# Performance work log

Hardware: AMD Instinct MI355X
Metric: run time of the kernel (lower is better)

The kernel has to match this reference:

```python
import jax, jax.numpy as jnp
import numpy as np


def setup_inputs() -> dict:
    key = jax.random.key(0)
    k1, k2, k3, k4 = jax.random.split(key, 4)
    N, T, F = 8192, 128, 9
    M_s = 256
    merged = jax.random.normal(k1, (N, T, F), dtype=jnp.float32)
    input1 = jax.random.normal(k2, (N, T, F), dtype=jnp.float32)
    samples = jax.random.normal(k3, (N, M_s), dtype=jnp.float32)
    labels = jax.random.randint(k4, (N,), 0, 10, dtype=jnp.int32)
    return {"merged": merged, "input1": input1, "samples": samples, "labels": labels}


def reference(merged, input1, samples, labels):
    # Pairwise squared distances S_ij = sum_k (s_i - s_j)^2 / M_s, computed via
    # the Gram-matrix identity instead of materializing the [N, N, M_s] tensor.
    M_s = samples.shape[1]
    sq = jnp.sum(samples * samples, axis=-1)                 # [N]
    gram = jnp.einsum('im,jm->ij', samples, samples)         # [N, N]
    S_ij = (sq[:, None] + sq[None, :] - 2.0 * gram) / jnp.float32(M_s)
    same = (labels[:, None] == labels[None, :]).astype(jnp.float32)
    term2 = jnp.mean(jnp.maximum(0.0, (1.0 - same) * (1.0 - S_ij)))
    L_label = 10.0 * jnp.mean(same * S_ij) + 10.0 * term2
    return L_label
```

## Files before the change

kernel.cpp:

```cpp
#include <hip/hip_runtime.h>
#include <hip/hip_bf16.h>

#define NROWS 8192
#define KDIM  256
#define NT    64
#define NBLK  (NT * (NT + 1) / 2)
#define GRID  256

typedef __attribute__((ext_vector_type(4))) float f32x4;

#define GLD(gp, lp)                                                            \
  __builtin_amdgcn_global_load_lds(                                            \
      (const __attribute__((address_space(1))) void*)(gp),                     \
      (__attribute__((address_space(3))) void*)(lp), 16, 0, 0)

__global__ void prep_kernel(const float* __restrict__ samples,
                            unsigned char* __restrict__ sf8,
                            float* __restrict__ sq,
                            float* __restrict__ accg) {
  int row = blockIdx.x, t = threadIdx.x;
  float2 v2 = ((const float2*)samples)[(size_t)row * 128 + t];
  int pk = __builtin_amdgcn_cvt_pk_fp8_f32(v2.x, v2.y, 0, false);
  ((unsigned short*)sf8)[(size_t)row * 128 + t] = (unsigned short)(pk & 0xffff);
  float p = v2.x * v2.x + v2.y * v2.y;
#pragma unroll
  for (int off = 32; off; off >>= 1) p += __shfl_down(p, off);
  __shared__ float ws2[2];
  if ((t & 63) == 0) ws2[t >> 6] = p;
  __syncthreads();
  if (t == 0) sq[row] = ws2[0] + ws2[1];
  if (row == 0 && t < 2) accg[t] = 0.0f;
}

__device__ inline void decode_tile(int b, int& bi, int& bj) {
  float disc = (2.0f * NT + 1.0f) * (2.0f * NT + 1.0f) - 8.0f * (float)b;
  bi = (int)(((2.0f * NT + 1.0f) - sqrtf(disc)) * 0.5f);
  if (bi < 0) bi = 0;
  if (bi > NT - 1) bi = NT - 1;
  while (bi > 0 && (bi * NT - bi * (bi - 1) / 2) > b) --bi;
  while (((bi + 1) * NT - (bi + 1) * bi / 2) <= b) ++bi;
  bj = bi + (b - (bi * NT - bi * (bi - 1) / 2));
}

__global__ __launch_bounds__(512, 1) void pair_kernel(
    const unsigned char* __restrict__ sf8, const float* __restrict__ sq,
    const int* __restrict__ labels, float* __restrict__ accg) {

  __shared__ __align__(16) unsigned char As[2][128 * 256];
  __shared__ __align__(16) unsigned char Bs[2][128 * 256];
  __shared__ float red[16];

  int t = threadIdx.x;
  int lane = t & 63;
  int w = t >> 6;
  int wm = w >> 1, wn = w & 1;
  int lr = lane >> 4, pc = lane & 15;
  int r = lane & 15;
  int kq = (lane >> 4) >> 1;
  int hf = ((lane >> 4) & 1) * 8;
  int q4 = (lane >> 4) * 4;
  int cl = lane & 15;

  float s1t = 0.f, s2t = 0.f;

  auto stage = [&](int bi_, int bj_, int buf) {
    int rA = bi_ * 128, rB = bj_ * 128;
#pragma unroll
    for (int p = 0; p < 4; ++p) {
      int region = p * 8 + w;
      int rr = region * 4 + lr;
      int c = pc ^ (rr & 15);
      GLD(sf8 + (size_t)(rA + rr) * KDIM + c * 16, &As[buf][region * 1024]);
      GLD(sf8 + (size_t)(rB + rr) * KDIM + c * 16, &Bs[buf][region * 1024]);
    }
  };

  int tile = blockIdx.x;
  int bi, bj;
  decode_tile(tile, bi, bj);
  stage(bi, bj, 0);
  int cur = 0;

  while (tile < NBLK) {
    int ntile = tile + GRID;
    int nbi = 0, nbj = 0;
    bool have_next = ntile < NBLK;
    if (have_next) decode_tile(ntile, nbi, nbj);

    __syncthreads();

    int rowA0 = bi * 128, rowB0 = bj * 128;
    float sqa[8], sqb[4];
    int laa[8], lab[4];
#pragma unroll
    for (int i = 0; i < 2; i++)
#pragma unroll
      for (int q = 0; q < 4; q++) {
        int gr = rowA0 + wm * 32 + i * 16 + q4 + q;
        sqa[i * 4 + q] = sq[gr];
        laa[i * 4 + q] = labels[gr];
      }
#pragma unroll
    for (int j = 0; j < 4; j++) {
      int gc = rowB0 + wn * 64 + j * 16 + cl;
      sqb[j] = sq[gc];
      lab[j] = labels[gc];
    }

    if (have_next) stage(nbi, nbj, cur ^ 1);

    f32x4 acc[2][4];
#pragma unroll
    for (int i = 0; i < 2; i++)
#pragma unroll
      for (int j = 0; j < 4; j++) acc[i][j] = (f32x4){0.f, 0.f, 0.f, 0.f};

#pragma unroll
    for (int kc = 0; kc < 8; ++kc) {
      long af[2], bfr[4];
#pragma unroll
      for (int i = 0; i < 2; i++) {
        int m = wm * 32 + i * 16 + r;
        af[i] = *(const long*)(&As[cur][m * 256 + (((kc * 2 + kq) ^ r) * 16) + hf]);
      }
#pragma unroll
      for (int j = 0; j < 4; j++) {
        int n = wn * 64 + j * 16 + r;
        bfr[j] = *(const long*)(&Bs[cur][n * 256 + (((kc * 2 + kq) ^ r) * 16) + hf]);
      }
#pragma unroll
      for (int i = 0; i < 2; i++)
#pragma unroll
        for (int j = 0; j < 4; j++)
          acc[i][j] = __builtin_amdgcn_mfma_f32_16x16x32_fp8_fp8(
              af[i], bfr[j], acc[i][j], 0, 0, 0);
    }

    float s1 = 0.f, s2 = 0.f;
#pragma unroll
    for (int j = 0; j < 4; j++) {
#pragma unroll
      for (int i = 0; i < 2; i++) {
#pragma unroll
        for (int q = 0; q < 4; q++) {
          float S = (sqa[i * 4 + q] + sqb[j] - 2.0f * acc[i][j][q]) *
                    (1.0f / 256.0f);
          if (laa[i * 4 + q] == lab[j]) s1 += S;
          else                          s2 += fmaxf(0.f, 1.f - S);
        }
      }
    }
    float wt = (bi == bj) ? 1.0f : 2.0f;
    s1t += wt * s1;
    s2t += wt * s2;

    tile = ntile; bi = nbi; bj = nbj; cur ^= 1;
  }

#pragma unroll
  for (int off = 32; off; off >>= 1) {
    s1t += __shfl_down(s1t, off);
    s2t += __shfl_down(s2t, off);
  }
  if (lane == 0) { red[w] = s1t; red[8 + w] = s2t; }
  __syncthreads();
  if (t == 0) {
    float a = 0.f, b2 = 0.f;
#pragma unroll
    for (int k = 0; k < 8; k++) { a += red[k]; b2 += red[8 + k]; }
    atomicAdd(&accg[0], a);
    atomicAdd(&accg[1], b2);
  }
}

__global__ void finalize_kernel(const float* __restrict__ accg,
                                float* __restrict__ out) {
  out[0] = 10.0f * (accg[0] + accg[1]) *
           (1.0f / ((float)NROWS * (float)NROWS));
}

extern "C" void kernel_launch(void* const* d_in, const int* in_sizes, int n_in,
                              void* d_out, int out_size, void* d_ws,
                              size_t ws_size, hipStream_t stream) {
  const float* samples = (const float*)d_in[2];
  const int*   labels  = (const int*)d_in[3];

  char* ws = (char*)d_ws;
  unsigned char* sf8 = (unsigned char*)ws;
  float* sq   = (float*)(ws + (size_t)NROWS * KDIM);
  float* accg = (float*)(ws + (size_t)NROWS * KDIM + NROWS * 4);
  float* out  = (float*)d_out;

  prep_kernel<<<NROWS, 128, 0, stream>>>(samples, sf8, sq, accg);
  pair_kernel<<<GRID, 512, 0, stream>>>(sf8, sq, labels, accg);
  finalize_kernel<<<1, 1, 0, stream>>>(accg, out);
}
```

Before: 136.1 us.

## Assign contiguous tile ranges per block and keep A operand in registers

```diff
diff --git a/kernel.cpp b/kernel.cpp
--- a/kernel.cpp
+++ b/kernel.cpp
@@ -5,7 +5,7 @@
 #define KDIM  256
 #define NT    64
 #define NBLK  (NT * (NT + 1) / 2)
-#define GRID  256
+#define GRID  512
 
 typedef __attribute__((ext_vector_type(4))) float f32x4;
 
@@ -18,18 +18,18 @@
                             unsigned char* __restrict__ sf8,
                             float* __restrict__ sq,
                             float* __restrict__ accg) {
-  int row = blockIdx.x, t = threadIdx.x;
-  float2 v2 = ((const float2*)samples)[(size_t)row * 128 + t];
-  int pk = __builtin_amdgcn_cvt_pk_fp8_f32(v2.x, v2.y, 0, false);
-  ((unsigned short*)sf8)[(size_t)row * 128 + t] = (unsigned short)(pk & 0xffff);
-  float p = v2.x * v2.x + v2.y * v2.y;
+  int t = threadIdx.x, lane = t & 63, wv = t >> 6;
+  int row = blockIdx.x * 4 + wv;
+  float4 v = ((const float4*)samples)[(size_t)row * 64 + lane];
+  int pk0 = __builtin_amdgcn_cvt_pk_fp8_f32(v.x, v.y, 0, false);
+  int pk1 = __builtin_amdgcn_cvt_pk_fp8_f32(v.z, v.w, 0, false);
+  ((unsigned int*)sf8)[(size_t)row * 64 + lane] =
+      (unsigned)(pk0 & 0xffff) | ((unsigned)pk1 << 16);
+  float p = v.x * v.x + v.y * v.y + v.z * v.z + v.w * v.w;
 #pragma unroll
   for (int off = 32; off; off >>= 1) p += __shfl_down(p, off);
-  __shared__ float ws2[2];
-  if ((t & 63) == 0) ws2[t >> 6] = p;
-  __syncthreads();
-  if (t == 0) sq[row] = ws2[0] + ws2[1];
-  if (row == 0 && t < 2) accg[t] = 0.0f;
+  if (lane == 0) sq[row] = p;
+  if (row == 0 && lane < 2) accg[lane] = 0.0f;
 }
 
 __device__ inline void decode_tile(int b, int& bi, int& bj) {
@@ -42,12 +42,11 @@
   bj = bi + (b - (bi * NT - bi * (bi - 1) / 2));
 }
 
-__global__ __launch_bounds__(512, 1) void pair_kernel(
+__global__ __launch_bounds__(512, 4) void pair_kernel(
     const unsigned char* __restrict__ sf8, const float* __restrict__ sq,
     const int* __restrict__ labels, float* __restrict__ accg) {
 
-  __shared__ __align__(16) unsigned char As[2][128 * 256];
-  __shared__ __align__(16) unsigned char Bs[2][128 * 256];
+  __shared__ __align__(16) unsigned char Bs[2][32 * 1024];
   __shared__ float red[16];
 
   int t = threadIdx.x;
@@ -56,58 +55,70 @@
   int wm = w >> 1, wn = w & 1;
   int lr = lane >> 4, pc = lane & 15;
   int r = lane & 15;
-  int kq = (lane >> 4) >> 1;
-  int hf = ((lane >> 4) & 1) * 8;
-  int q4 = (lane >> 4) * 4;
-  int cl = lane & 15;
-
-  float s1t = 0.f, s2t = 0.f;
-
-  auto stage = [&](int bi_, int bj_, int buf) {
-    int rA = bi_ * 128, rB = bj_ * 128;
+  int ko = lane >> 4;
+  int kq = ko >> 1, hf = (ko & 1) * 8;
+  int q4 = ko * 4;
+
+  int t0 = (blockIdx.x * 65) >> 4;
+  int t1 = ((blockIdx.x + 1) * 65) >> 4;
+  int bi, bj;
+  decode_tile(t0, bi, bj);
+
+  long af[2][8];
+  float sqa[8];
+  int laa[8];
+  auto loadA = [&](int bi_) {
+#pragma unroll
+    for (int i = 0; i < 2; i++) {
+      const unsigned char* Ar =
+          sf8 + (size_t)(bi_ * 128 + wm * 32 + i * 16 + r) * KDIM + ko * 8;
+#pragma unroll
+      for (int kc = 0; kc < 8; kc++) af[i][kc] = *(const long*)(Ar + kc * 32);
+    }
+#pragma unroll
+    for (int i = 0; i < 2; i++)
+#pragma unroll
+      for (int q = 0; q < 4; q++) {
+        int gr = bi_ * 128 + wm * 32 + i * 16 + q4 + q;
+        sqa[i * 4 + q] = sq[gr];
+        laa[i * 4 + q] = labels[gr];
+      }
+  };
+
+  auto stageB = [&](int bj_, int buf) {
 #pragma unroll
     for (int p = 0; p < 4; ++p) {
       int region = p * 8 + w;
       int rr = region * 4 + lr;
       int c = pc ^ (rr & 15);
-      GLD(sf8 + (size_t)(rA + rr) * KDIM + c * 16, &As[buf][region * 1024]);
-      GLD(sf8 + (size_t)(rB + rr) * KDIM + c * 16, &Bs[buf][region * 1024]);
+      GLD(sf8 + (size_t)(bj_ * 128 + rr) * KDIM + c * 16,
+          &Bs[buf][region * 1024]);
     }
   };
 
-  int tile = blockIdx.x;
-  int bi, bj;
-  decode_tile(tile, bi, bj);
-  stage(bi, bj, 0);
+  int abi = bi;
+  loadA(bi);
+  stageB(bj, 0);
   int cur = 0;
-
-  while (tile < NBLK) {
-    int ntile = tile + GRID;
-    int nbi = 0, nbj = 0;
-    bool have_next = ntile < NBLK;
-    if (have_next) decode_tile(ntile, nbi, nbj);
-
+  float s1t = 0.f, s2t = 0.f;
+
+  for (int tile = t0; tile < t1; ++tile) {
     __syncthreads();
 
-    int rowA0 = bi * 128, rowB0 = bj * 128;
-    float sqa[8], sqb[4];
-    int laa[8], lab[4];
-#pragma unroll
-    for (int i = 0; i < 2; i++)
-#pragma unroll
-      for (int q = 0; q < 4; q++) {
-        int gr = rowA0 + wm * 32 + i * 16 + q4 + q;
-        sqa[i * 4 + q] = sq[gr];
-        laa[i * 4 + q] = labels[gr];
-      }
+    float sqb[4];
+    int lab[4];
 #pragma unroll
     for (int j = 0; j < 4; j++) {
-      int gc = rowB0 + wn * 64 + j * 16 + cl;
+      int gc = bj * 128 + wn * 64 + j * 16 + r;
       sqb[j] = sq[gc];
       lab[j] = labels[gc];
     }
 
-    if (have_next) stage(nbi, nbj, cur ^ 1);
+    if (bi != abi) { loadA(bi); abi = bi; }
+
+    int nbi = bi, nbj = bj + 1;
+    if (nbj == NT) { ++nbi; nbj = nbi; }
+    if (tile + 1 < t1) stageB(nbj, cur ^ 1);
 
     f32x4 acc[2][4];
 #pragma unroll
@@ -117,23 +128,19 @@
 
 #pragma unroll
     for (int kc = 0; kc < 8; ++kc) {
-      long af[2], bfr[4];
-#pragma unroll
-      for (int i = 0; i < 2; i++) {
-        int m = wm * 32 + i * 16 + r;
-        af[i] = *(const long*)(&As[cur][m * 256 + (((kc * 2 + kq) ^ r) * 16) + hf]);
-      }
+      long bfr[4];
 #pragma unroll
       for (int j = 0; j < 4; j++) {
         int n = wn * 64 + j * 16 + r;
-        bfr[j] = *(const long*)(&Bs[cur][n * 256 + (((kc * 2 + kq) ^ r) * 16) + hf]);
+        bfr[j] =
+            *(const long*)(&Bs[cur][n * 256 + (((kc * 2 + kq) ^ r) * 16) + hf]);
       }
 #pragma unroll
       for (int i = 0; i < 2; i++)
 #pragma unroll
         for (int j = 0; j < 4; j++)
           acc[i][j] = __builtin_amdgcn_mfma_f32_16x16x32_fp8_fp8(
-              af[i], bfr[j], acc[i][j], 0, 0, 0);
+              af[i][kc], bfr[j], acc[i][j], 0, 0, 0);
     }
 
     float s1 = 0.f, s2 = 0.f;
@@ -154,7 +161,7 @@
     s1t += wt * s1;
     s2t += wt * s2;
 
-    tile = ntile; bi = nbi; bj = nbj; cur ^= 1;
+    bi = nbi; bj = nbj; cur ^= 1;
   }
 
 #pragma unroll
@@ -191,7 +198,7 @@
   float* accg = (float*)(ws + (size_t)NROWS * KDIM + NROWS * 4);
   float* out  = (float*)d_out;
 
-  prep_kernel<<<NROWS, 128, 0, stream>>>(samples, sf8, sq, accg);
+  prep_kernel<<<NROWS / 4, 256, 0, stream>>>(samples, sf8, sq, accg);
   pair_kernel<<<GRID, 512, 0, stream>>>(sf8, sq, labels, accg);
   finalize_kernel<<<1, 1, 0, stream>>>(accg, out);
 }
```

After: 153.0 us. 12.4% more time.
